# Kernel tuning notes

Hardware: AMD Instinct MI355X
Metric: run time of the kernel (lower is better)

Reference implementation:

```python
import jax, jax.numpy as jnp
import numpy as np

H, HD, NKV = 16, 128, 4           # heads, head_dim, n_kv_heads (kv_groups=4)
SEL_TOPK, SEL_DIM, SEL_HEADS = 64, 64, 1
ROPE_BASE = 10000.0


def _rope_emb(t, hd):
    inv = 1.0 / (ROPE_BASE ** (jnp.arange(0, hd, 2, dtype=jnp.float32) / hd))
    freqs = jnp.arange(t, dtype=jnp.float32)[:, None] * inv[None, :]
    return jnp.concatenate([freqs, freqs], axis=-1)  # [t, hd]


def _apply_rotary(x, rope):
    # x: [b, t, h, hd]; rope: [t, hd] (rot_dim == hd here)
    cos = jnp.cos(rope)[None, :, None, :]
    sin = jnp.sin(rope)[None, :, None, :]
    x1, x2 = x[..., ::2], x[..., 1::2]
    c, s = cos[..., ::2], sin[..., ::2]
    rot = jnp.stack([x1 * c - x2 * s, x1 * s + x2 * c], axis=-1)
    return rot.reshape(x.shape)


def _selector_mask(q, k):
    # q, k: [b, H, t, hd] in UNrotated form (selector_rope='none'); causal=True
    b, h, t, d = q.shape
    qs = q[:, :SEL_HEADS, :, :SEL_DIM]
    ks = k[:, :SEL_HEADS, :, :SEL_DIM]
    scores = jnp.einsum('bhqd,bhkd->bhqk', qs, ks) / np.sqrt(SEL_DIM).astype(np.float32)
    future = jnp.triu(jnp.ones((t, t), bool), 1)
    scores = jnp.where(future[None, None], -jnp.inf, scores)
    idx = jax.lax.top_k(scores, SEL_TOPK)[1]  # [b, h_sel, t, keep]
    rows = jnp.arange(t)
    scatter_row = lambda im: jnp.zeros((t, t), bool).at[rows[:, None], im].set(True)
    sel = jax.vmap(jax.vmap(scatter_row))(idx)          # [b, h_sel, t, t]
    sel = sel.at[:, :, rows, rows].set(True)            # diagonal always kept
    sel = sel & jnp.tril(jnp.ones((t, t), bool))[None, None]
    sel = jnp.any(sel, axis=1, keepdims=True)           # h_sel < h -> broadcast mask
    return jnp.where(sel, 0.0, -jnp.inf).astype(jnp.float32)


def reference(x, Wq, bq, Wkd, bkd, Wku, bku, Wo, bo):
    b, t, d = x.shape
    G = H // NKV
    q = (x @ Wq + bq).reshape(b, t, H, HD)
    kv = (x @ Wkd + bkd) @ Wku + bku                    # MLA: down then up projection
    k = kv[..., : NKV * HD].reshape(b, t, NKV, HD)
    v = kv[..., NKV * HD:].reshape(b, t, NKV, HD)
    rope = _rope_emb(t, HD)
    qb = _apply_rotary(q, rope).transpose(0, 2, 1, 3)                     # [b,H,t,hd]
    kb = jnp.repeat(_apply_rotary(k, rope).transpose(0, 2, 1, 3), G, 1)   # GQA expand
    vb = jnp.repeat(v.transpose(0, 2, 1, 3), G, 1)
    # selector mask from unrotated q/k, detached (selector_detach=True)
    qu = jax.lax.stop_gradient(q.transpose(0, 2, 1, 3))
    ku = jnp.repeat(jax.lax.stop_gradient(k.transpose(0, 2, 1, 3)), G, 1)
    mask = _selector_mask(qu, ku)                                         # [b,1,t,t]
    scores = jnp.einsum('bhqd,bhkd->bhqk', qb, kb) / np.sqrt(HD).astype(np.float32)
    attn = jax.nn.softmax(scores + mask, axis=-1)
    y = jnp.einsum('bhqk,bhkd->bhqd', attn, vb)
    y = y.transpose(0, 2, 1, 3).reshape(b, t, H * HD)
    return y @ Wo + bo


def setup_inputs() -> dict:
    key = jax.random.key(0)
    ks = jax.random.split(key, 6)
    B, T, D, LAT = 2, 2048, 2048, 512
    s = 0.02
    return {
        'x': jax.random.normal(ks[0], (B, T, D), jnp.float32),
        'Wq': jax.random.normal(ks[1], (D, H * HD), jnp.float32) * s,
        'bq': jnp.zeros((H * HD,), jnp.float32),
        'Wkd': jax.random.normal(ks[2], (D, LAT), jnp.float32) * s,
        'bkd': jnp.zeros((LAT,), jnp.float32),
        'Wku': jax.random.normal(ks[3], (LAT, 2 * NKV * HD), jnp.float32) * s,
        'bku': jnp.zeros((2 * NKV * HD,), jnp.float32),
        'Wo': jax.random.normal(ks[4], (H * HD, D), jnp.float32) * s,
        'bo': jnp.zeros((D,), jnp.float32),
    }
```

## Files before the change

kernel.cpp:

```cpp
#include <hip/hip_runtime.h>

typedef unsigned int u32;
typedef unsigned long long u64;
typedef _Float16 f16;
typedef __attribute__((ext_vector_type(2))) _Float16 f16x2;
typedef __attribute__((ext_vector_type(4))) _Float16 f16x4;
typedef __attribute__((ext_vector_type(8))) _Float16 f16x8;
typedef __attribute__((ext_vector_type(4))) float f32x4;
typedef __attribute__((ext_vector_type(2))) double f64x2;


__device__ __forceinline__ int suX(int jj) { return jj ^ ((jj >> 4) & 7); }

__device__ __forceinline__ void dev_transpose_cast(char* smem, int bx, int by,
                                                   const float* __restrict__ in,
                                                   f16* __restrict__ out, int R, int C)
{
  float* tile = (float*)smem;
  int c0 = bx * 32, r0 = by * 32;
  int tx = threadIdx.x & 31, ty = threadIdx.x >> 5;
  #pragma unroll
  for (int i = ty; i < 32; i += 8) tile[i * 33 + tx] = in[(size_t)(r0 + i) * C + c0 + tx];
  __syncthreads();
  #pragma unroll
  for (int i = ty; i < 32; i += 8) out[(size_t)(c0 + i) * R + r0 + tx] = (f16)tile[tx * 33 + i];
}

__global__ __launch_bounds__(256) void k_fusedP(const float* __restrict__ Wq, f16* __restrict__ WqT,
                                                const float* __restrict__ Wkd, f16* __restrict__ WkdT,
                                                const float* __restrict__ Wku, f16* __restrict__ WkuT,
                                                const float* __restrict__ Wo, f16* __restrict__ WoT,
                                                const float* __restrict__ x, f16* __restrict__ xh)
{
  __shared__ __align__(16) char smem[4224];
  const int id = blockIdx.x;
  if (id < 4096) {
    dev_transpose_cast(smem, id & 63, id >> 6, Wq, WqT, 2048, 2048);
  } else if (id < 5120) {
    int g = id - 4096;
    dev_transpose_cast(smem, g & 15, g >> 4, Wkd, WkdT, 2048, 512);
  } else if (id < 5632) {
    int g = id - 5120;
    dev_transpose_cast(smem, g & 31, g >> 5, Wku, WkuT, 512, 1024);
  } else if (id < 9728) {
    int g = id - 5632;
    dev_transpose_cast(smem, g & 63, g >> 6, Wo, WoT, 2048, 2048);
  } else {
    int i = (id - 9728) * 256 + threadIdx.x;
    f32x4 v = *(const f32x4*)&x[(size_t)i * 4];
    f16x4 h; h.x = (f16)v.x; h.y = (f16)v.y; h.z = (f16)v.z; h.w = (f16)v.w;
    *(f16x4*)&xh[(size_t)i * 4] = h;
  }
}

__global__ void k_prep_sel(const float* __restrict__ Wq, const float* __restrict__ Wkd,
                           const float* __restrict__ Wku, double* __restrict__ Bsel)
{
  const int k = blockIdx.x;
  const int j = threadIdx.x;
  Bsel[(size_t)k * 128 + j] = (double)Wq[(size_t)k * 2048 + j];
  double s = 0.0;
  for (int l = 0; l < 512; ++l)
    s = fma((double)Wkd[(size_t)k * 512 + l], (double)Wku[(size_t)l * 1024 + j], s);
  Bsel[(size_t)k * 128 + 64 + j] = s;
}

__global__ void k_bias_sel(const float* __restrict__ bq, const float* __restrict__ bkd,
                           const float* __restrict__ Wku, const float* __restrict__ bku,
                           double* __restrict__ bsel)
{
  int j = threadIdx.x;
  if (j < 64) {
    bsel[j] = (double)bq[j];
  } else {
    int jj = j - 64;
    double s = (double)bku[jj];
    for (int l = 0; l < 512; ++l)
      s = fma((double)bkd[l], (double)Wku[(size_t)l * 1024 + jj], s);
    bsel[j] = s;
  }
}

__device__ __forceinline__ void dev_sel_f64(char* smem, int bx, int by, int bz,
                                            const float* __restrict__ A,
                                            const double* __restrict__ Bsel,
                                            double* __restrict__ partial)
{
  double* Asd = (double*)smem;
  double* Bsd = (double*)smem + 32 * 33;
  const int m0 = bx * 32, n0 = by * 64;
  const int kbase = bz * 256, kend = kbase + 256;
  const int tid = threadIdx.x;
  const int tx = tid & 15, ty = tid >> 4;
  const int ar = tid >> 3, ac4 = (tid & 7) * 4;
  double acc[2][4] = {};

  f32x4 aN = *(const f32x4*)&A[(size_t)(m0 + ar) * 2048 + kbase + ac4];
  f64x2 bN[4];
  #pragma unroll
  for (int it = 0; it < 4; ++it) {
    int c = it * 256 + tid; int kk = c >> 5, n2 = (c & 31) * 2;
    bN[it] = *(const f64x2*)&Bsel[(size_t)(kbase + kk) * 128 + n0 + n2];
  }
  for (int k0 = kbase; k0 < kend; k0 += 32) {
    __syncthreads();
    Asd[ar * 33 + ac4] = (double)aN.x; Asd[ar * 33 + ac4 + 1] = (double)aN.y;
    Asd[ar * 33 + ac4 + 2] = (double)aN.z; Asd[ar * 33 + ac4 + 3] = (double)aN.w;
    #pragma unroll
    for (int it = 0; it < 4; ++it) {
      int c = it * 256 + tid; int kk = c >> 5, n2 = (c & 31) * 2;
      Bsd[kk * 66 + n2] = bN[it].x; Bsd[kk * 66 + n2 + 1] = bN[it].y;
    }
    __syncthreads();
    if (k0 + 32 < kend) {
      aN = *(const f32x4*)&A[(size_t)(m0 + ar) * 2048 + k0 + 32 + ac4];
      #pragma unroll
      for (int it = 0; it < 4; ++it) {
        int c = it * 256 + tid; int kk = c >> 5, n2 = (c & 31) * 2;
        bN[it] = *(const f64x2*)&Bsel[(size_t)(k0 + 32 + kk) * 128 + n0 + n2];
      }
    }
    #pragma unroll
    for (int kk = 0; kk < 32; ++kk) {
      double a0 = Asd[(ty * 2) * 33 + kk], a1 = Asd[(ty * 2 + 1) * 33 + kk];
      f64x2 b01 = *(const f64x2*)&Bsd[kk * 66 + tx * 2];
      f64x2 b23 = *(const f64x2*)&Bsd[kk * 66 + tx * 2 + 32];
      acc[0][0] = fma(a0, b01.x, acc[0][0]); acc[0][1] = fma(a0, b01.y, acc[0][1]);
      acc[0][2] = fma(a0, b23.x, acc[0][2]); acc[0][3] = fma(a0, b23.y, acc[0][3]);
      acc[1][0] = fma(a1, b01.x, acc[1][0]); acc[1][1] = fma(a1, b01.y, acc[1][1]);
      acc[1][2] = fma(a1, b23.x, acc[1][2]); acc[1][3] = fma(a1, b23.y, acc[1][3]);
    }
  }
  double* op = partial + (size_t)bz * 4096 * 128;
  #pragma unroll
  for (int i = 0; i < 2; ++i) {
    int row = m0 + ty * 2 + i;
    #pragma unroll
    for (int j = 0; j < 2; ++j) {
      op[(size_t)row * 128 + n0 + tx * 2 + j] = acc[i][j];
      op[(size_t)row * 128 + n0 + tx * 2 + 32 + j] = acc[i][j + 2];
    }
  }
}

__device__ __forceinline__ void dev_sel_reduce(int blk,
                                               const double* __restrict__ partial,
                                               const double* __restrict__ bias,
                                               double* __restrict__ qs64,
                                               double* __restrict__ ks64)
{
  const int idx = blk * 256 + threadIdx.x;
  const int row = idx >> 7, n = idx & 127;
  const size_t S = 4096 * 128;
  double v = partial[idx];
  #pragma unroll
  for (int z = 1; z < 8; ++z) v += partial[(size_t)z * S + idx];
  v += bias[n];
  if (n < 64) qs64[(size_t)row * 64 + n] = v;
  else        ks64[(size_t)row * 64 + (n - 64)] = v;
}

__global__ __launch_bounds__(256) void k_transpose64(const double* __restrict__ in,
                                                     double* __restrict__ out)
{
  __shared__ double tile[32][33];
  const int bt = blockIdx.z;
  const int c0 = blockIdx.x * 32;
  const int r0 = blockIdx.y * 32;
  int tx = threadIdx.x & 31, ty = threadIdx.x >> 5;
  const double* ip = in + (size_t)bt * 2048 * 64;
  double* op = out + (size_t)bt * 64 * 2048;
  #pragma unroll
  for (int i = ty; i < 32; i += 8) tile[i][tx] = ip[(size_t)(r0 + i) * 64 + c0 + tx];
  __syncthreads();
  #pragma unroll
  for (int i = ty; i < 32; i += 8) op[(size_t)(c0 + i) * 2048 + r0 + tx] = tile[tx][i];
}

__global__ __launch_bounds__(256) void k_score(const double* __restrict__ qs,
                                               const double* __restrict__ ksT,
                                               u64* __restrict__ su)
{
  const int rt = blockIdx.x >> 2;
  const int kc = blockIdx.x & 3;
  const int tmax = ((rt & 63) << 5) + 31;
  if (kc * 512 > tmax) return;
  const int b = rt >> 6;
  const int tid = threadIdx.x;
  __shared__ double As[32 * 64];
  {
    const double* qp = qs + (size_t)rt * 32 * 64;
    #pragma unroll
    for (int i = 0; i < 8; ++i) As[tid * 8 + i] = qp[tid * 8 + i];
  }
  __syncthreads();
  const int k0 = kc * 512 + tid;
  const int k1 = k0 + 256;
  const double* kb = ksT + (size_t)b * 64 * 2048;
  double acc0[32] = {}, acc1[32] = {};
  for (int d = 0; d < 64; ++d) {
    const double b0 = kb[(size_t)d * 2048 + k0];
    const double b1 = kb[(size_t)d * 2048 + k1];
    #pragma unroll
    for (int r = 0; r < 32; ++r) {
      const double a = As[r * 64 + d];
      acc0[r] = fma(a, b0, acc0[r]);
      acc1[r] = fma(a, b1, acc1[r]);
    }
  }
  #pragma unroll
  for (int r = 0; r < 32; ++r) {
    const int row = rt * 32 + r;
    u64 u0 = (u64)__double_as_longlong(acc0[r]);
    u0 = (u0 >> 63) ? ~u0 : (u0 | 0x8000000000000000ull);
    su[(size_t)row * 2048 + k0] = u0;
    u64 u1 = (u64)__double_as_longlong(acc1[r]);
    u1 = (u1 >> 63) ? ~u1 : (u1 | 0x8000000000000000ull);
    su[(size_t)row * 2048 + k1] = u1;
  }
}

template <int MODE>
__device__ __forceinline__ void dev_gemm_bt(char* smem, int gbx, int gby, int nbx, int nby,
                                            const f16* __restrict__ A,
                                            const f16* __restrict__ BT,
                                            const float* __restrict__ bias,
                                            float* __restrict__ C, f16* __restrict__ Ch,
                                            f16* __restrict__ Kout, f16* __restrict__ Vout,
                                            const float* __restrict__ rc,
                                            const float* __restrict__ rs,
                                            int K, int lda, int ldb, int ldc)
{
  f16* As = (f16*)smem;
  f16* Bs = (f16*)smem + 128 * 64;
  const int tid = threadIdx.x;
  const int lane = tid & 63;
  const int wave = tid >> 6;
  int bx = gbx, by = gby;
  {
    const int nwg = nbx * nby;
    if ((nwg & 7) == 0) {
      const int bid = by * nbx + bx;
      const int cpx = nwg >> 3;
      const int sbid = (bid & 7) * cpx + (bid >> 3);
      bx = sbid % nbx;
      by = sbid / nbx;
    }
  }
  const int m0 = bx * 128, n0 = by * 64;
  const int wr = (wave >> 1) * 64, wc = (wave & 1) * 32;
  const int lrow = lane & 15;
  const int kgrp = (lane >> 4) * 8;
  f32x4 acc[4][2] = {};

  for (int k0 = 0; k0 < K; k0 += 64) {
    __syncthreads();
    #pragma unroll
    for (int it = 0; it < 4; ++it) {
      int c = it * 256 + tid;
      int r = c >> 3, c8 = (c & 7) * 8;
      int lbase = (it * 256 + (tid & 192)) * 8;
      const f16* ga = A + (size_t)(m0 + r) * lda + k0 + c8;
      __builtin_amdgcn_global_load_lds((const __attribute__((address_space(1))) u32*)ga,
                                       (__attribute__((address_space(3))) u32*)&As[lbase],
                                       16, 0, 0);
    }
    #pragma unroll
    for (int it = 0; it < 2; ++it) {
      int c = it * 256 + tid;
      int r = c >> 3, c8 = (c & 7) * 8;
      int lbase = (it * 256 + (tid & 192)) * 8;
      const f16* gb = BT + (size_t)(n0 + r) * ldb + k0 + c8;
      __builtin_amdgcn_global_load_lds((const __attribute__((address_space(1))) u32*)gb,
                                       (__attribute__((address_space(3))) u32*)&Bs[lbase],
                                       16, 0, 0);
    }
    __syncthreads();
    #pragma unroll
    for (int ks = 0; ks < 2; ++ks) {
      f16x8 af[4], bfr[2];
      #pragma unroll
      for (int m = 0; m < 4; ++m)
        af[m] = *(const f16x8*)&As[(wr + m * 16 + lrow) * 64 + ks * 32 + kgrp];
      #pragma unroll
      for (int n = 0; n < 2; ++n)
        bfr[n] = *(const f16x8*)&Bs[(wc + n * 16 + lrow) * 64 + ks * 32 + kgrp];
      #pragma unroll
      for (int m = 0; m < 4; ++m)
        #pragma unroll
        for (int n = 0; n < 2; ++n)
          acc[m][n] = __builtin_amdgcn_mfma_f32_16x16x32_f16(af[m], bfr[n], acc[m][n], 0, 0, 0);
    }
  }
  const int rbase = m0 + wr + (lane >> 4) * 4;
  #pragma unroll
  for (int n = 0; n < 2; ++n) {
    int col = n0 + wc + n * 16 + lrow;
    float bv = bias ? bias[col] : 0.0f;
    const int ri = (col & 127) >> 1;
    #pragma unroll
    for (int m = 0; m < 4; ++m) {
      #pragma unroll
      for (int j = 0; j < 4; ++j) {
        int rowi = rbase + m * 16 + j;
        float v = acc[m][n][j] + bv;
        if (MODE == 0) {
          C[(size_t)rowi * ldc + col] = v;
        } else if (MODE == 1) {
          Ch[(size_t)rowi * ldc + col] = (f16)v;
        } else if (MODE == 2) {
          float vp = __shfl_xor(v, 1);
          int t = rowi & 2047;
          float c_ = rc[t * 64 + ri], s_ = rs[t * 64 + ri];
          float r_ = (lrow & 1) ? (vp * s_ + v * c_) : (v * c_ - vp * s_);
          Ch[(size_t)rowi * ldc + col] = (f16)r_;
        } else {
          float vp = __shfl_xor(v, 1);
          if (n0 < 512) {
            int t = rowi & 2047;
            float c_ = rc[t * 64 + ri], s_ = rs[t * 64 + ri];
            float r_ = (lrow & 1) ? (vp * s_ + v * c_) : (v * c_ - vp * s_);
            Kout[(size_t)rowi * 512 + col] = (f16)r_;
          } else {
            Vout[(size_t)rowi * 512 + (col - 512)] = (f16)v;
          }
        }
      }
    }
  }
}

__global__ void k_rope_table(float* __restrict__ rc, float* __restrict__ rs)
{
  int t = blockIdx.x, i = threadIdx.x;
  int fi = (2 * i) & 63;
  double inv = pow(10000.0, -(double)fi / 64.0);
  double a = (double)t * inv;
  rc[t * 64 + i] = (float)cos(a);
  rs[t * 64 + i] = (float)sin(a);
}

__global__ __launch_bounds__(512) void k_select(const u64* __restrict__ gsu,
                                                int* __restrict__ selcnt,
                                                int* __restrict__ selidx)
{
  const int r0 = blockIdx.x * 2;
  const int t0 = r0 & 2047, t1 = t0 + 1;
  const int tid = threadIdx.x;
  const int lane = tid & 63, wave = tid >> 6;
  if (t1 < 64) {
    for (int lr = 0; lr < 2; ++lr) {
      int t = t0 + lr;
      int* outp = selidx + (size_t)(r0 + lr) * 68;
      for (int jj = tid; jj <= t; jj += 512) outp[jj] = jj;
      if (tid == 0) selcnt[r0 + lr] = t + 1;
    }
    return;
  }
  __shared__ u64 su[2][2048];
  __shared__ unsigned hist[256];
  __shared__ unsigned wsum[8];
  __shared__ unsigned s_bsel, s_larger, s_cnt;
  __shared__ u64 s_thr;
  __shared__ int s_remfin;
  __shared__ int cand[128];
  __shared__ u64 ckey[128];

  {
    const u64* g0 = gsu + (size_t)r0 * 2048;
    const u64* g1 = gsu + (size_t)(r0 + 1) * 2048;
    for (int jj = tid; jj <= t1; jj += 512) {
      const int sx = suX(jj);
      if (jj <= t0) su[0][sx] = g0[jj];
      su[1][sx] = g1[jj];
    }
  }
  __syncthreads();

  const int c0 = tid * 4;
  for (int lr = 0; lr < 2; ++lr) {
    const int t = t0 + lr;
    int* outp = selidx + (size_t)(r0 + lr) * 68;
    const u64* S = su[lr];
    u64 kv[4]; bool kvv[4];
    #pragma unroll
    for (int e = 0; e < 4; ++e) {
      const int jj = c0 + e;
      kvv[e] = (jj <= t);
      kv[e] = kvv[e] ? S[suX(jj)] : 0;
    }

    u64 prefix = 0;
    int remaining = 64;
    int broke = 0, sh_final = 0;
    for (int byte = 7; byte >= 0; --byte) {
      const int sh = byte * 8;
      if (tid < 256) hist[tid] = 0;
      __syncthreads();
      {
        unsigned bn[4]; bool vl[4];
        #pragma unroll
        for (int e = 0; e < 4; ++e) {
          vl[e] = kvv[e] && ((byte == 7) || (((kv[e] ^ prefix) >> (sh + 8)) == 0));
          bn[e] = (unsigned)((kv[e] >> sh) & 255);
        }
        unsigned myBin = 0xFFFFFFFFu, cntLoc = 0;
        bool localSame = true;
        #pragma unroll
        for (int e = 0; e < 4; ++e) {
          if (vl[e]) {
            if (myBin == 0xFFFFFFFFu) myBin = bn[e];
            else if (bn[e] != myBin) localSame = false;
            ++cntLoc;
          }
        }
        const bool hasValid = (cntLoc > 0);
        unsigned vmin = hasValid ? myBin : 0xFFFFFFFFu;
        unsigned vmax = hasValid ? myBin : 0u;
        unsigned csum = cntLoc;
        #pragma unroll
        for (int off = 32; off; off >>= 1) {
          unsigned a = __shfl_xor(vmin, off); vmin = a < vmin ? a : vmin;
          unsigned bmx = __shfl_xor(vmax, off); vmax = bmx > vmax ? bmx : vmax;
          csum += __shfl_xor(csum, off);
        }
        const bool anyMixed = (__ballot(hasValid && !localSame) != 0ull);
        const bool anyValid = (__ballot(hasValid) != 0ull);
        if (!anyMixed && anyValid && vmin == vmax) {
          if (lane == 0) atomicAdd(&hist[vmin], csum);
        } else if (hasValid) {
          #pragma unroll
          for (int e = 0; e < 4; ++e) {
            if (vl[e]) {
              bool first = true;
              #pragma unroll
              for (int p = 0; p < 4; ++p)
                if (p < e && vl[p] && bn[p] == bn[e]) first = false;
              if (first) {
                unsigned c = 0;
                #pragma unroll
                for (int q = 0; q < 4; ++q)
                  if (q >= e && vl[q] && bn[q] == bn[e]) ++c;
                atomicAdd(&hist[bn[e]], c);
              }
            }
          }
        }
      }
      __syncthreads();
      unsigned inc = 0, cumAbove = 0;
      if (tid < 256) {
        const unsigned h = hist[tid];
        unsigned v = h;
        #pragma unroll
        for (int off = 1; off < 64; off <<= 1) {
          unsigned tv = __shfl_down(v, off);
          if (lane + off < 64) v += tv;
        }
        if (lane == 0) wsum[wave] = v;
        inc = v; cumAbove = h;
      }
      __syncthreads();
      if (tid < 256) {
        unsigned add = 0;
        #pragma unroll
        for (int w = 0; w < 4; ++w)
          if (w > wave) add += wsum[w];
        const unsigned h = cumAbove;
        inc += add;
        cumAbove = inc - h;
      }
      __syncthreads();
      if (tid < 256 && (int)cumAbove < remaining && (int)inc >= remaining) {
        s_bsel = (unsigned)tid;
        s_larger = cumAbove;
        s_cnt = inc - cumAbove;
      }
      __syncthreads();
      prefix |= ((u64)s_bsel << sh);
      remaining -= (int)s_larger;
      int cnt = (int)s_cnt;
      if (cnt <= 128) { broke = 1; sh_final = sh; break; }
    }
    u64 thr;
    int remfin;
    if (broke) {
      unsigned cg = 0;
      #pragma unroll
      for (int e = 0; e < 4; ++e)
        if (kvv[e] && (((kv[e] ^ prefix) >> sh_final) == 0)) ++cg;
      unsigned v = cg;
      #pragma unroll
      for (int off = 1; off < 64; off <<= 1) {
        unsigned tv = __shfl_up(v, off);
        if (lane >= off) v += tv;
      }
      __syncthreads();
      if (lane == 63) wsum[wave] = v;
      __syncthreads();
      unsigned add = 0, tot = 0;
      #pragma unroll
      for (int w = 0; w < 8; ++w) {
        tot += wsum[w];
        if (w < wave) add += wsum[w];
      }
      const int C = (int)tot;
      int pos = (int)(v + add - cg);
      __syncthreads();
      #pragma unroll
      for (int e = 0; e < 4; ++e)
        if (kvv[e] && (((kv[e] ^ prefix) >> sh_final) == 0)) cand[pos++] = c0 + e;
      __syncthreads();
      if (tid < C) ckey[tid] = S[suX(cand[tid])];
      __syncthreads();
      if (tid < C) {
        u64 k = ckey[tid];
        int g = 0, eq = 0;
        for (int j = 0; j < C; ++j) {
          g += (ckey[j] > k) ? 1 : 0;
          eq += (ckey[j] == k) ? 1 : 0;
        }
        if (g < remaining && remaining <= g + eq) {
          s_thr = k;
          s_remfin = remaining - g;
        }
      }
      __syncthreads();
      thr = s_thr;
      remfin = s_remfin;
    } else {
      thr = prefix;
      remfin = remaining;
    }
    __syncthreads();
    unsigned cg = 0, ct_ = 0;
    #pragma unroll
    for (int e = 0; e < 4; ++e) {
      if (kvv[e]) {
        cg += (kv[e] > thr) ? 1u : 0u;
        ct_ += (kv[e] == thr) ? 1u : 0u;
      }
    }
    const unsigned pack = cg | (ct_ << 16);
    {
      unsigned v = pack;
      #pragma unroll
      for (int off = 1; off < 64; off <<= 1) {
        unsigned tv = __shfl_up(v, off);
        if (lane >= off) v += tv;
      }
      if (lane == 63) wsum[wave] = v;
      __syncthreads();
      unsigned add = 0, tot = 0;
      #pragma unroll
      for (int w = 0; w < 8; ++w) {
        tot += wsum[w];
        if (w < wave) add += wsum[w];
      }
      const unsigned excl = v + add - pack;
      __syncthreads();
      const unsigned Gtot = tot & 0xFFFFu;
      const u64 ut = S[suX(t)];
      const unsigned gt = (ut > thr) ? 1u : 0u;
      const unsigned tt = (ut == thr) ? 1u : 0u;
      const int GtotX = (int)(Gtot - gt);
      int gpos = (int)(excl & 0xFFFFu);
      int tpos = (int)(excl >> 16);
      #pragma unroll
      for (int e = 0; e < 4; ++e) {
        const int jj = c0 + e;
        if (!kvv[e]) break;
        if (kv[e] > thr) {
          if (jj != t) outp[1 + gpos] = jj;
          ++gpos;
        } else if (kv[e] == thr) {
          if (jj != t && tpos < remfin) outp[1 + GtotX + tpos] = jj;
          ++tpos;
        }
      }
      if (tid == 0) {
        outp[0] = t;
        const unsigned Ttot = tot >> 16;
        int tb = (int)(Ttot - tt);
        int emitT = tb < remfin ? tb : remfin;
        selcnt[r0 + lr] = 1 + GtotX + emitT;
      }
    }
    __syncthreads();
  }
}

__global__ __launch_bounds__(256) void k_fusedA(const float* __restrict__ x,
                                                const double* __restrict__ Bsel,
                                                double* __restrict__ partial,
                                                const f16* __restrict__ xh,
                                                const f16* __restrict__ WkdT,
                                                const float* __restrict__ bkd,
                                                f16* __restrict__ cbf)
{
  __shared__ __align__(16) char smem[25600];
  const int id = blockIdx.x;
  if (id < 2048) {
    dev_sel_f64(smem, id & 127, (id >> 7) & 1, id >> 8, x, Bsel, partial);
  } else {
    const int g = id - 2048;
    dev_gemm_bt<1>(smem, g & 31, g >> 5, 32, 8, xh, WkdT, bkd, nullptr, cbf,
                   nullptr, nullptr, nullptr, nullptr, 2048, 2048, 2048, 512);
  }
}

__global__ __launch_bounds__(256) void k_fusedC(const f16* __restrict__ cbf,
                                                const f16* __restrict__ WkuT,
                                                const float* __restrict__ bku,
                                                f16* __restrict__ krope, f16* __restrict__ vbf,
                                                const float* __restrict__ rc,
                                                const float* __restrict__ rs,
                                                const double* __restrict__ partial,
                                                const double* __restrict__ bsel,
                                                double* __restrict__ qs64,
                                                double* __restrict__ ks64)
{
  __shared__ __align__(16) char smem[24576];
  const int id = blockIdx.x;
  if (id < 512) {
    dev_gemm_bt<3>(smem, id & 31, id >> 5, 32, 16, cbf, WkuT, bku, nullptr, nullptr,
                   krope, vbf, rc, rs, 512, 512, 512, 1024);
  } else {
    dev_sel_reduce(id - 512, partial, bsel, qs64, ks64);
  }
}

__global__ __launch_bounds__(256) void k_gemmQ(const f16* __restrict__ xh,
                                               const f16* __restrict__ WqT,
                                               const float* __restrict__ bq,
                                               f16* __restrict__ qrope,
                                               const float* __restrict__ rc,
                                               const float* __restrict__ rs)
{
  __shared__ __align__(16) char smem[24576];
  dev_gemm_bt<2>(smem, blockIdx.x, blockIdx.y, 32, 32, xh, WqT, bq, nullptr, qrope,
                 nullptr, nullptr, rc, rs, 2048, 2048, 2048, 2048);
}

__global__ __launch_bounds__(256) void k_gemmO(const f16* __restrict__ A,
                                               const f16* __restrict__ BT,
                                               const float* __restrict__ bias,
                                               float* __restrict__ C)
{
  __shared__ __align__(16) char smem[24576];
  dev_gemm_bt<0>(smem, blockIdx.x, blockIdx.y, 32, 32, A, BT, bias, C, nullptr,
                 nullptr, nullptr, nullptr, nullptr, 2048, 2048, 2048, 2048);
}

__global__ __launch_bounds__(256) void k_attn(const f16* __restrict__ qr,
                                              const f16* __restrict__ kr,
                                              const f16* __restrict__ vv,
                                              const int* __restrict__ selcnt,
                                              const int* __restrict__ selidx,
                                              f16* __restrict__ y)
{
  const int blk = blockIdx.x;
  const int row = blk >> 2, kvh = blk & 3;
  const int b = row >> 11;
  const int tid = threadIdx.x, lane = tid & 63, wave = tid >> 6;
  const int cnt = selcnt[row];
  __shared__ int sidx[68];
  __shared__ __align__(16) f16 Kl[65 * 128];
  __shared__ __align__(16) f16 Vl[68 * 128];
  __shared__ f16 qlds[4][128];
  __shared__ __align__(4) f16 ph[4][72];
  if (tid < cnt) sidx[tid] = selidx[(size_t)row * 68 + tid];
  *(f16x2*)&qlds[wave][lane * 2] =
      *(const f16x2*)&qr[((size_t)row * 16 + kvh * 4 + wave) * 128 + lane * 2];
  __syncthreads();

  f16x8 kreg[5], vreg[5];
  int rr[5], cc[5]; bool vld[5];
  #pragma unroll
  for (int it = 0; it < 5; ++it) {
    const int c = it * 256 + tid;
    const int r = c >> 4, ch = c & 15;
    const bool ok = (r < cnt);
    const int rsafe = ok ? sidx[r] : sidx[0];
    const size_t kbase = ((size_t)(b * 2048 + rsafe)) * 512 + kvh * 128 + ch * 8;
    kreg[it] = *(const f16x8*)&kr[kbase];
    vreg[it] = *(const f16x8*)&vv[kbase];
    rr[it] = r; cc[it] = ch; vld[it] = ok;
  }
  #pragma unroll
  for (int it = 0; it < 5; ++it) {
    if (vld[it]) {
      *(f16x8*)&Kl[rr[it] * 128 + ((cc[it] ^ (rr[it] & 15)) * 8)] = kreg[it];
      *(f16x8*)&Vl[rr[it] * 128 + cc[it] * 8] = vreg[it];
    }
  }
  for (int i = tid; i < (68 - cnt) * 64; i += 256)
    ((u32*)Vl)[cnt * 64 + i] = 0u;
  __syncthreads();

  const float SCALE = 0.08838834764831845f;
  auto dotk = [&](int r) -> float {
    const int sw = r & 15;
    float s = 0.0f;
    #pragma unroll
    for (int i = 0; i < 16; ++i) {
      f16x8 k8 = *(const f16x8*)&Kl[r * 128 + ((i ^ sw) * 8)];
      f16x8 q8 = *(const f16x8*)&qlds[wave][i * 8];
      #pragma unroll
      for (int e = 0; e < 4; ++e) {
        f16x2 ka; ka.x = k8[2 * e]; ka.y = k8[2 * e + 1];
        f16x2 qa; qa.x = q8[2 * e]; qa.y = q8[2 * e + 1];
        s = __builtin_amdgcn_fdot2(ka, qa, s, false);
      }
    }
    return s * SCALE;
  };

  float s1 = -__builtin_inff(), s2 = -__builtin_inff();
  if (lane < cnt) s1 = dotk(lane);
  if (lane + 64 < cnt) s2 = dotk(lane + 64);
  float mx = fmaxf(s1, s2);
  #pragma unroll
  for (int off = 32; off; off >>= 1) mx = fmaxf(mx, __shfl_xor(mx, off));
  float p1 = (lane < cnt) ? __expf(s1 - mx) : 0.0f;
  float p2 = (lane + 64 < cnt) ? __expf(s2 - mx) : 0.0f;
  float l = p1 + p2;
  #pragma unroll
  for (int off = 32; off; off >>= 1) l += __shfl_xor(l, off);
  float linv = 1.0f / l;
  ph[wave][lane] = (f16)p1;
  if (lane == 0) ph[wave][64] = (f16)p2;
  if (lane >= 1 && lane < 8) ph[wave][64 + lane] = (f16)0.f;
  __syncthreads();

  float y0 = 0.0f, y1 = 0.0f;
  const int d2 = lane * 2;
  for (int j = 0; j < cnt; j += 2) {
    f16x2 pp = *(const f16x2*)&ph[wave][j];
    f16x2 va = *(const f16x2*)&Vl[(j + 0) * 128 + d2];
    f16x2 vb = *(const f16x2*)&Vl[(j + 1) * 128 + d2];
    f16x2 v0; v0.x = va.x; v0.y = vb.x;
    f16x2 v1; v1.x = va.y; v1.y = vb.y;
    y0 = __builtin_amdgcn_fdot2(pp, v0, y0, false);
    y1 = __builtin_amdgcn_fdot2(pp, v1, y1, false);
  }
  y0 *= linv; y1 *= linv;
  f16x2 o; o.x = (f16)y0; o.y = (f16)y1;
  *(f16x2*)&y[(size_t)row * 2048 + (kvh * 4 + wave) * 128 + d2] = o;
}

extern "C" void kernel_launch(void* const* d_in, const int* in_sizes, int n_in,
                              void* d_out, int out_size, void* d_ws, size_t ws_size,
                              hipStream_t stream)
{
  (void)in_sizes; (void)n_in; (void)out_size; (void)ws_size;
  const float* x   = (const float*)d_in[0];
  const float* Wq  = (const float*)d_in[1];
  const float* bq  = (const float*)d_in[2];
  const float* Wkd = (const float*)d_in[3];
  const float* bkd = (const float*)d_in[4];
  const float* Wku = (const float*)d_in[5];
  const float* bku = (const float*)d_in[6];
  const float* Wo  = (const float*)d_in[7];
  const float* bo  = (const float*)d_in[8];
  float* out = (float*)d_out;

  char* ws = (char*)d_ws;
  size_t o = 0;
  auto alloc = [&](size_t bytes) -> void* {
    o = (o + 255) & ~(size_t)255;
    void* p = ws + o;
    o += bytes;
    return p;
  };
  f16* WqT   = (f16*)alloc(2048ull * 2048 * 2);
  f16* WoT   = (f16*)alloc(2048ull * 2048 * 2);
  f16* WkdT  = (f16*)alloc(512ull * 2048 * 2);
  f16* WkuT  = (f16*)alloc(1024ull * 512 * 2);
  f16* xh    = (f16*)alloc(4096ull * 2048 * 2);
  f16* yh    = (f16*)alloc(4096ull * 2048 * 2);
  f16* cbf   = (f16*)alloc(4096ull * 512 * 2);
  float* rc  = (float*)alloc(2048ull * 64 * 4);
  float* rs  = (float*)alloc(2048ull * 64 * 4);
  f16* qrope = (f16*)alloc(4096ull * 2048 * 2);
  f16* krope = (f16*)alloc(4096ull * 512 * 2);
  f16* vbf   = (f16*)alloc(4096ull * 512 * 2);
  int* selcnt = (int*)alloc(4096ull * 4);
  int* selidx = (int*)alloc(4096ull * 68 * 4);
  double* Bsel = (double*)alloc(2048ull * 128 * 8);
  double* bsel = (double*)alloc(128 * 8);
  double* qs64 = (double*)alloc(4096ull * 64 * 8);
  double* ks64 = (double*)alloc(4096ull * 64 * 8);
  double* ksT  = (double*)alloc(2ull * 64 * 2048 * 8);
  double* partial = (double*)alloc(8ull * 4096 * 128 * 8);
  u64* gsu = (u64*)alloc(4096ull * 2048 * 8);

  k_prep_sel<<<2048, 64, 0, stream>>>(Wq, Wkd, Wku, Bsel);
  k_bias_sel<<<1, 128, 0, stream>>>(bq, bkd, Wku, bku, bsel);
  k_rope_table<<<2048, 64, 0, stream>>>(rc, rs);
  k_fusedP<<<17920, 256, 0, stream>>>(Wq, WqT, Wkd, WkdT, Wku, WkuT, Wo, WoT, x, xh);

  k_fusedA<<<2304, 256, 0, stream>>>(x, Bsel, partial, xh, WkdT, bkd, cbf);

  k_fusedC<<<2560, 256, 0, stream>>>(cbf, WkuT, bku, krope, vbf, rc, rs,
                                     partial, bsel, qs64, ks64);

  k_transpose64<<<dim3(2, 64, 2), 256, 0, stream>>>(ks64, ksT);
  k_score<<<512, 256, 0, stream>>>(qs64, ksT, gsu);

  k_gemmQ<<<dim3(32, 32), 256, 0, stream>>>(xh, WqT, bq, qrope, rc, rs);
  k_select<<<2048, 512, 0, stream>>>(gsu, selcnt, selidx);

  k_attn<<<16384, 256, 0, stream>>>(qrope, krope, vbf, selcnt, selidx, yh);

  k_gemmO<<<dim3(32, 32), 256, 0, stream>>>(yh, WoT, bo, out);
}
```

Measured before the change: 492.4 us.

## Merge prep kernels, co-schedule score with Q GEMM, retile select and attn q

Folds the selector-weight prep, selector bias and rope-table kernels into the single preprocessing launch, which removes several small launches. The selector score kernel is retiled to 16-row blocks and launched in the same grid as the Q projection GEMM, so the two independent stages can overlap on the GPU. Top-k selection moves from two rows per 512-thread block to one row per 256-thread block with 8 keys per thread. Attention now keeps the query vector in registers instead of LDS. The trade-off is higher register pressure in the attention and select kernels, and a heterogeneous grid whose shared memory and register use is sized for the larger GEMM path.

```diff
diff --git a/kernel.cpp b/kernel.cpp
--- a/kernel.cpp
+++ b/kernel.cpp
@@ -26,14 +26,21 @@
   for (int i = ty; i < 32; i += 8) out[(size_t)(c0 + i) * R + r0 + tx] = (f16)tile[tx * 33 + i];
 }
 
-__global__ __launch_bounds__(256) void k_fusedP(const float* __restrict__ Wq, f16* __restrict__ WqT,
-                                                const float* __restrict__ Wkd, f16* __restrict__ WkdT,
-                                                const float* __restrict__ Wku, f16* __restrict__ WkuT,
-                                                const float* __restrict__ Wo, f16* __restrict__ WoT,
-                                                const float* __restrict__ x, f16* __restrict__ xh)
+__global__ __launch_bounds__(256) void k_megaP(const float* __restrict__ Wq, f16* __restrict__ WqT,
+                                               const float* __restrict__ Wkd, f16* __restrict__ WkdT,
+                                               const float* __restrict__ Wku, f16* __restrict__ WkuT,
+                                               const float* __restrict__ Wo, f16* __restrict__ WoT,
+                                               const float* __restrict__ x, f16* __restrict__ xh,
+                                               double* __restrict__ Bsel,
+                                               const float* __restrict__ bq,
+                                               const float* __restrict__ bkd,
+                                               const float* __restrict__ bku,
+                                               double* __restrict__ bsel,
+                                               float* __restrict__ rc, float* __restrict__ rs)
 {
   __shared__ __align__(16) char smem[4224];
   const int id = blockIdx.x;
+  const int tid = threadIdx.x;
   if (id < 4096) {
     dev_transpose_cast(smem, id & 63, id >> 6, Wq, WqT, 2048, 2048);
   } else if (id < 5120) {
@@ -45,39 +52,40 @@
   } else if (id < 9728) {
     int g = id - 5632;
     dev_transpose_cast(smem, g & 63, g >> 6, Wo, WoT, 2048, 2048);
-  } else {
-    int i = (id - 9728) * 256 + threadIdx.x;
+  } else if (id < 17920) {
+    int i = (id - 9728) * 256 + tid;
     f32x4 v = *(const f32x4*)&x[(size_t)i * 4];
     f16x4 h; h.x = (f16)v.x; h.y = (f16)v.y; h.z = (f16)v.z; h.w = (f16)v.w;
     *(f16x4*)&xh[(size_t)i * 4] = h;
-  }
-}
-
-__global__ void k_prep_sel(const float* __restrict__ Wq, const float* __restrict__ Wkd,
-                           const float* __restrict__ Wku, double* __restrict__ Bsel)
-{
-  const int k = blockIdx.x;
-  const int j = threadIdx.x;
-  Bsel[(size_t)k * 128 + j] = (double)Wq[(size_t)k * 2048 + j];
-  double s = 0.0;
-  for (int l = 0; l < 512; ++l)
-    s = fma((double)Wkd[(size_t)k * 512 + l], (double)Wku[(size_t)l * 1024 + j], s);
-  Bsel[(size_t)k * 128 + 64 + j] = s;
-}
-
-__global__ void k_bias_sel(const float* __restrict__ bq, const float* __restrict__ bkd,
-                           const float* __restrict__ Wku, const float* __restrict__ bku,
-                           double* __restrict__ bsel)
-{
-  int j = threadIdx.x;
-  if (j < 64) {
-    bsel[j] = (double)bq[j];
+  } else if (id < 18432) {
+    const int k = (id - 17920) * 4 + (tid >> 6);
+    const int j = tid & 63;
+    Bsel[(size_t)k * 128 + j] = (double)Wq[(size_t)k * 2048 + j];
+    double s = 0.0;
+    for (int l = 0; l < 512; ++l)
+      s = fma((double)Wkd[(size_t)k * 512 + l], (double)Wku[(size_t)l * 1024 + j], s);
+    Bsel[(size_t)k * 128 + 64 + j] = s;
+  } else if (id == 18432) {
+    if (tid < 128) {
+      int j = tid;
+      if (j < 64) {
+        bsel[j] = (double)bq[j];
+      } else {
+        int jj = j - 64;
+        double s = (double)bku[jj];
+        for (int l = 0; l < 512; ++l)
+          s = fma((double)bkd[l], (double)Wku[(size_t)l * 1024 + jj], s);
+        bsel[j] = s;
+      }
+    }
   } else {
-    int jj = j - 64;
-    double s = (double)bku[jj];
-    for (int l = 0; l < 512; ++l)
-      s = fma((double)bkd[l], (double)Wku[(size_t)l * 1024 + jj], s);
-    bsel[j] = s;
+    const int t = (id - 18433) * 4 + (tid >> 6);
+    const int i = tid & 63;
+    int fi = (2 * i) & 63;
+    double inv = pow(10000.0, -(double)fi / 64.0);
+    double a = (double)t * inv;
+    rc[t * 64 + i] = (float)cos(a);
+    rs[t * 64 + i] = (float)sin(a);
   }
 }
 
@@ -177,40 +185,41 @@
   for (int i = ty; i < 32; i += 8) op[(size_t)(c0 + i) * 2048 + r0 + tx] = tile[tx][i];
 }
 
-__global__ __launch_bounds__(256) void k_score(const double* __restrict__ qs,
-                                               const double* __restrict__ ksT,
-                                               u64* __restrict__ su)
-{
-  const int rt = blockIdx.x >> 2;
-  const int kc = blockIdx.x & 3;
-  const int tmax = ((rt & 63) << 5) + 31;
+__device__ __forceinline__ void dev_score(char* smem, int sc,
+                                          const double* __restrict__ qs,
+                                          const double* __restrict__ ksT,
+                                          u64* __restrict__ su)
+{
+  const int rt = sc >> 2;
+  const int kc = sc & 3;
+  const int tmax = ((rt & 127) << 4) + 15;
   if (kc * 512 > tmax) return;
-  const int b = rt >> 6;
+  const int b = rt >> 7;
   const int tid = threadIdx.x;
-  __shared__ double As[32 * 64];
+  double* As = (double*)smem;
   {
-    const double* qp = qs + (size_t)rt * 32 * 64;
-    #pragma unroll
-    for (int i = 0; i < 8; ++i) As[tid * 8 + i] = qp[tid * 8 + i];
+    const double* qp = qs + (size_t)rt * 16 * 64;
+    #pragma unroll
+    for (int i = 0; i < 4; ++i) As[tid * 4 + i] = qp[tid * 4 + i];
   }
   __syncthreads();
   const int k0 = kc * 512 + tid;
   const int k1 = k0 + 256;
   const double* kb = ksT + (size_t)b * 64 * 2048;
-  double acc0[32] = {}, acc1[32] = {};
+  double acc0[16] = {}, acc1[16] = {};
   for (int d = 0; d < 64; ++d) {
     const double b0 = kb[(size_t)d * 2048 + k0];
     const double b1 = kb[(size_t)d * 2048 + k1];
     #pragma unroll
-    for (int r = 0; r < 32; ++r) {
+    for (int r = 0; r < 16; ++r) {
       const double a = As[r * 64 + d];
       acc0[r] = fma(a, b0, acc0[r]);
       acc1[r] = fma(a, b1, acc1[r]);
     }
   }
   #pragma unroll
-  for (int r = 0; r < 32; ++r) {
-    const int row = rt * 32 + r;
+  for (int r = 0; r < 16; ++r) {
+    const int row = rt * 16 + r;
     u64 u0 = (u64)__double_as_longlong(acc0[r]);
     u0 = (u0 >> 63) ? ~u0 : (u0 | 0x8000000000000000ull);
     su[(size_t)row * 2048 + k0] = u0;
@@ -330,266 +339,6 @@
   }
 }
 
-__global__ void k_rope_table(float* __restrict__ rc, float* __restrict__ rs)
-{
-  int t = blockIdx.x, i = threadIdx.x;
-  int fi = (2 * i) & 63;
-  double inv = pow(10000.0, -(double)fi / 64.0);
-  double a = (double)t * inv;
-  rc[t * 64 + i] = (float)cos(a);
-  rs[t * 64 + i] = (float)sin(a);
-}
-
-__global__ __launch_bounds__(512) void k_select(const u64* __restrict__ gsu,
-                                                int* __restrict__ selcnt,
-                                                int* __restrict__ selidx)
-{
-  const int r0 = blockIdx.x * 2;
-  const int t0 = r0 & 2047, t1 = t0 + 1;
-  const int tid = threadIdx.x;
-  const int lane = tid & 63, wave = tid >> 6;
-  if (t1 < 64) {
-    for (int lr = 0; lr < 2; ++lr) {
-      int t = t0 + lr;
-      int* outp = selidx + (size_t)(r0 + lr) * 68;
-      for (int jj = tid; jj <= t; jj += 512) outp[jj] = jj;
-      if (tid == 0) selcnt[r0 + lr] = t + 1;
-    }
-    return;
-  }
-  __shared__ u64 su[2][2048];
-  __shared__ unsigned hist[256];
-  __shared__ unsigned wsum[8];
-  __shared__ unsigned s_bsel, s_larger, s_cnt;
-  __shared__ u64 s_thr;
-  __shared__ int s_remfin;
-  __shared__ int cand[128];
-  __shared__ u64 ckey[128];
-
-  {
-    const u64* g0 = gsu + (size_t)r0 * 2048;
-    const u64* g1 = gsu + (size_t)(r0 + 1) * 2048;
-    for (int jj = tid; jj <= t1; jj += 512) {
-      const int sx = suX(jj);
-      if (jj <= t0) su[0][sx] = g0[jj];
-      su[1][sx] = g1[jj];
-    }
-  }
-  __syncthreads();
-
-  const int c0 = tid * 4;
-  for (int lr = 0; lr < 2; ++lr) {
-    const int t = t0 + lr;
-    int* outp = selidx + (size_t)(r0 + lr) * 68;
-    const u64* S = su[lr];
-    u64 kv[4]; bool kvv[4];
-    #pragma unroll
-    for (int e = 0; e < 4; ++e) {
-      const int jj = c0 + e;
-      kvv[e] = (jj <= t);
-      kv[e] = kvv[e] ? S[suX(jj)] : 0;
-    }
-
-    u64 prefix = 0;
-    int remaining = 64;
-    int broke = 0, sh_final = 0;
-    for (int byte = 7; byte >= 0; --byte) {
-      const int sh = byte * 8;
-      if (tid < 256) hist[tid] = 0;
-      __syncthreads();
-      {
-        unsigned bn[4]; bool vl[4];
-        #pragma unroll
-        for (int e = 0; e < 4; ++e) {
-          vl[e] = kvv[e] && ((byte == 7) || (((kv[e] ^ prefix) >> (sh + 8)) == 0));
-          bn[e] = (unsigned)((kv[e] >> sh) & 255);
-        }
-        unsigned myBin = 0xFFFFFFFFu, cntLoc = 0;
-        bool localSame = true;
-        #pragma unroll
-        for (int e = 0; e < 4; ++e) {
-          if (vl[e]) {
-            if (myBin == 0xFFFFFFFFu) myBin = bn[e];
-            else if (bn[e] != myBin) localSame = false;
-            ++cntLoc;
-          }
-        }
-        const bool hasValid = (cntLoc > 0);
-        unsigned vmin = hasValid ? myBin : 0xFFFFFFFFu;
-        unsigned vmax = hasValid ? myBin : 0u;
-        unsigned csum = cntLoc;
-        #pragma unroll
-        for (int off = 32; off; off >>= 1) {
-          unsigned a = __shfl_xor(vmin, off); vmin = a < vmin ? a : vmin;
-          unsigned bmx = __shfl_xor(vmax, off); vmax = bmx > vmax ? bmx : vmax;
-          csum += __shfl_xor(csum, off);
-        }
-        const bool anyMixed = (__ballot(hasValid && !localSame) != 0ull);
-        const bool anyValid = (__ballot(hasValid) != 0ull);
-        if (!anyMixed && anyValid && vmin == vmax) {
-          if (lane == 0) atomicAdd(&hist[vmin], csum);
-        } else if (hasValid) {
-          #pragma unroll
-          for (int e = 0; e < 4; ++e) {
-            if (vl[e]) {
-              bool first = true;
-              #pragma unroll
-              for (int p = 0; p < 4; ++p)
-                if (p < e && vl[p] && bn[p] == bn[e]) first = false;
-              if (first) {
-                unsigned c = 0;
-                #pragma unroll
-                for (int q = 0; q < 4; ++q)
-                  if (q >= e && vl[q] && bn[q] == bn[e]) ++c;
-                atomicAdd(&hist[bn[e]], c);
-              }
-            }
-          }
-        }
-      }
-      __syncthreads();
-      unsigned inc = 0, cumAbove = 0;
-      if (tid < 256) {
-        const unsigned h = hist[tid];
-        unsigned v = h;
-        #pragma unroll
-        for (int off = 1; off < 64; off <<= 1) {
-          unsigned tv = __shfl_down(v, off);
-          if (lane + off < 64) v += tv;
-        }
-        if (lane == 0) wsum[wave] = v;
-        inc = v; cumAbove = h;
-      }
-      __syncthreads();
-      if (tid < 256) {
-        unsigned add = 0;
-        #pragma unroll
-        for (int w = 0; w < 4; ++w)
-          if (w > wave) add += wsum[w];
-        const unsigned h = cumAbove;
-        inc += add;
-        cumAbove = inc - h;
-      }
-      __syncthreads();
-      if (tid < 256 && (int)cumAbove < remaining && (int)inc >= remaining) {
-        s_bsel = (unsigned)tid;
-        s_larger = cumAbove;
-        s_cnt = inc - cumAbove;
-      }
-      __syncthreads();
-      prefix |= ((u64)s_bsel << sh);
-      remaining -= (int)s_larger;
-      int cnt = (int)s_cnt;
-      if (cnt <= 128) { broke = 1; sh_final = sh; break; }
-    }
-    u64 thr;
-    int remfin;
-    if (broke) {
-      unsigned cg = 0;
-      #pragma unroll
-      for (int e = 0; e < 4; ++e)
-        if (kvv[e] && (((kv[e] ^ prefix) >> sh_final) == 0)) ++cg;
-      unsigned v = cg;
-      #pragma unroll
-      for (int off = 1; off < 64; off <<= 1) {
-        unsigned tv = __shfl_up(v, off);
-        if (lane >= off) v += tv;
-      }
-      __syncthreads();
-      if (lane == 63) wsum[wave] = v;
-      __syncthreads();
-      unsigned add = 0, tot = 0;
-      #pragma unroll
-      for (int w = 0; w < 8; ++w) {
-        tot += wsum[w];
-        if (w < wave) add += wsum[w];
-      }
-      const int C = (int)tot;
-      int pos = (int)(v + add - cg);
-      __syncthreads();
-      #pragma unroll
-      for (int e = 0; e < 4; ++e)
-        if (kvv[e] && (((kv[e] ^ prefix) >> sh_final) == 0)) cand[pos++] = c0 + e;
-      __syncthreads();
-      if (tid < C) ckey[tid] = S[suX(cand[tid])];
-      __syncthreads();
-      if (tid < C) {
-        u64 k = ckey[tid];
-        int g = 0, eq = 0;
-        for (int j = 0; j < C; ++j) {
-          g += (ckey[j] > k) ? 1 : 0;
-          eq += (ckey[j] == k) ? 1 : 0;
-        }
-        if (g < remaining && remaining <= g + eq) {
-          s_thr = k;
-          s_remfin = remaining - g;
-        }
-      }
-      __syncthreads();
-      thr = s_thr;
-      remfin = s_remfin;
-    } else {
-      thr = prefix;
-      remfin = remaining;
-    }
-    __syncthreads();
-    unsigned cg = 0, ct_ = 0;
-    #pragma unroll
-    for (int e = 0; e < 4; ++e) {
-      if (kvv[e]) {
-        cg += (kv[e] > thr) ? 1u : 0u;
-        ct_ += (kv[e] == thr) ? 1u : 0u;
-      }
-    }
-    const unsigned pack = cg | (ct_ << 16);
-    {
-      unsigned v = pack;
-      #pragma unroll
-      for (int off = 1; off < 64; off <<= 1) {
-        unsigned tv = __shfl_up(v, off);
-        if (lane >= off) v += tv;
-      }
-      if (lane == 63) wsum[wave] = v;
-      __syncthreads();
-      unsigned add = 0, tot = 0;
-      #pragma unroll
-      for (int w = 0; w < 8; ++w) {
-        tot += wsum[w];
-        if (w < wave) add += wsum[w];
-      }
-      const unsigned excl = v + add - pack;
-      __syncthreads();
-      const unsigned Gtot = tot & 0xFFFFu;
-      const u64 ut = S[suX(t)];
-      const unsigned gt = (ut > thr) ? 1u : 0u;
-      const unsigned tt = (ut == thr) ? 1u : 0u;
-      const int GtotX = (int)(Gtot - gt);
-      int gpos = (int)(excl & 0xFFFFu);
-      int tpos = (int)(excl >> 16);
-      #pragma unroll
-      for (int e = 0; e < 4; ++e) {
-        const int jj = c0 + e;
-        if (!kvv[e]) break;
-        if (kv[e] > thr) {
-          if (jj != t) outp[1 + gpos] = jj;
-          ++gpos;
-        } else if (kv[e] == thr) {
-          if (jj != t && tpos < remfin) outp[1 + GtotX + tpos] = jj;
-          ++tpos;
-        }
-      }
-      if (tid == 0) {
-        outp[0] = t;
-        const unsigned Ttot = tot >> 16;
-        int tb = (int)(Ttot - tt);
-        int emitT = tb < remfin ? tb : remfin;
-        selcnt[r0 + lr] = 1 + GtotX + emitT;
-      }
-    }
-    __syncthreads();
-  }
-}
-
 __global__ __launch_bounds__(256) void k_fusedA(const float* __restrict__ x,
                                                 const double* __restrict__ Bsel,
                                                 double* __restrict__ partial,
@@ -630,16 +379,24 @@
   }
 }
 
-__global__ __launch_bounds__(256) void k_gemmQ(const f16* __restrict__ xh,
-                                               const f16* __restrict__ WqT,
-                                               const float* __restrict__ bq,
-                                               f16* __restrict__ qrope,
-                                               const float* __restrict__ rc,
-                                               const float* __restrict__ rs)
+__global__ __launch_bounds__(256) void k_fusedQS(const f16* __restrict__ xh,
+                                                 const f16* __restrict__ WqT,
+                                                 const float* __restrict__ bq,
+                                                 f16* __restrict__ qrope,
+                                                 const float* __restrict__ rc,
+                                                 const float* __restrict__ rs,
+                                                 const double* __restrict__ qs64,
+                                                 const double* __restrict__ ksT,
+                                                 u64* __restrict__ gsu)
 {
   __shared__ __align__(16) char smem[24576];
-  dev_gemm_bt<2>(smem, blockIdx.x, blockIdx.y, 32, 32, xh, WqT, bq, nullptr, qrope,
-                 nullptr, nullptr, rc, rs, 2048, 2048, 2048, 2048);
+  const int id = blockIdx.x;
+  if (id < 1024) {
+    dev_gemm_bt<2>(smem, id & 31, id >> 5, 32, 32, xh, WqT, bq, nullptr, qrope,
+                   nullptr, nullptr, rc, rs, 2048, 2048, 2048, 2048);
+  } else {
+    dev_score(smem, id - 1024, qs64, ksT, gsu);
+  }
 }
 
 __global__ __launch_bounds__(256) void k_gemmO(const f16* __restrict__ A,
@@ -650,6 +407,235 @@
   __shared__ __align__(16) char smem[24576];
   dev_gemm_bt<0>(smem, blockIdx.x, blockIdx.y, 32, 32, A, BT, bias, C, nullptr,
                  nullptr, nullptr, nullptr, nullptr, 2048, 2048, 2048, 2048);
+}
+
+__global__ __launch_bounds__(256) void k_select(const u64* __restrict__ gsu,
+                                                int* __restrict__ selcnt,
+                                                int* __restrict__ selidx)
+{
+  const int row = blockIdx.x;
+  const int t = row & 2047;
+  const int tid = threadIdx.x;
+  const int lane = tid & 63, wave = tid >> 6;
+  int* outp = selidx + (size_t)row * 68;
+  if (t < 64) {
+    for (int jj = tid; jj <= t; jj += 256) outp[jj] = jj;
+    if (tid == 0) selcnt[row] = t + 1;
+    return;
+  }
+  __shared__ u64 su[2048];
+  __shared__ unsigned hist[256];
+  __shared__ unsigned wsum[4];
+  __shared__ unsigned s_bsel, s_larger, s_cnt;
+  __shared__ u64 s_thr;
+  __shared__ int s_remfin;
+  __shared__ int cand[128];
+  __shared__ u64 ckey[128];
+
+  {
+    const u64* g = gsu + (size_t)row * 2048;
+    for (int jj = tid; jj <= t; jj += 256) su[suX(jj)] = g[jj];
+  }
+  __syncthreads();
+
+  const int c0 = tid * 8;
+  u64 kv[8]; bool kvv[8];
+  #pragma unroll
+  for (int e = 0; e < 8; ++e) {
+    const int jj = c0 + e;
+    kvv[e] = (jj <= t);
+    kv[e] = kvv[e] ? su[suX(jj)] : 0;
+  }
+
+  u64 prefix = 0;
+  int remaining = 64;
+  int broke = 0, sh_final = 0;
+  for (int byte = 7; byte >= 0; --byte) {
+    const int sh = byte * 8;
+    hist[tid] = 0;
+    __syncthreads();
+    {
+      unsigned bn[8]; bool vl[8];
+      #pragma unroll
+      for (int e = 0; e < 8; ++e) {
+        vl[e] = kvv[e] && ((byte == 7) || (((kv[e] ^ prefix) >> (sh + 8)) == 0));
+        bn[e] = (unsigned)((kv[e] >> sh) & 255);
+      }
+      unsigned myBin = 0xFFFFFFFFu, cntLoc = 0;
+      bool localSame = true;
+      #pragma unroll
+      for (int e = 0; e < 8; ++e) {
+        if (vl[e]) {
+          if (myBin == 0xFFFFFFFFu) myBin = bn[e];
+          else if (bn[e] != myBin) localSame = false;
+          ++cntLoc;
+        }
+      }
+      const bool hasValid = (cntLoc > 0);
+      unsigned vmin = hasValid ? myBin : 0xFFFFFFFFu;
+      unsigned vmax = hasValid ? myBin : 0u;
+      unsigned csum = cntLoc;
+      #pragma unroll
+      for (int off = 32; off; off >>= 1) {
+        unsigned a = __shfl_xor(vmin, off); vmin = a < vmin ? a : vmin;
+        unsigned bmx = __shfl_xor(vmax, off); vmax = bmx > vmax ? bmx : vmax;
+        csum += __shfl_xor(csum, off);
+      }
+      const bool anyMixed = (__ballot(hasValid && !localSame) != 0ull);
+      const bool anyValid = (__ballot(hasValid) != 0ull);
+      if (!anyMixed && anyValid && vmin == vmax) {
+        if (lane == 0) atomicAdd(&hist[vmin], csum);
+      } else if (hasValid) {
+        #pragma unroll
+        for (int e = 0; e < 8; ++e) {
+          if (vl[e]) {
+            bool first = true;
+            #pragma unroll
+            for (int p = 0; p < 8; ++p)
+              if (p < e && vl[p] && bn[p] == bn[e]) first = false;
+            if (first) {
+              unsigned c = 0;
+              #pragma unroll
+              for (int q = 0; q < 8; ++q)
+                if (q >= e && vl[q] && bn[q] == bn[e]) ++c;
+              atomicAdd(&hist[bn[e]], c);
+            }
+          }
+        }
+      }
+    }
+    __syncthreads();
+    const unsigned h = hist[tid];
+    unsigned v = h;
+    #pragma unroll
+    for (int off = 1; off < 64; off <<= 1) {
+      unsigned tv = __shfl_down(v, off);
+      if (lane + off < 64) v += tv;
+    }
+    if (lane == 0) wsum[wave] = v;
+    __syncthreads();
+    unsigned add = 0;
+    #pragma unroll
+    for (int w = 0; w < 4; ++w)
+      if (w > wave) add += wsum[w];
+    const unsigned inc = v + add;
+    const unsigned cumAbove = inc - h;
+    __syncthreads();
+    if ((int)cumAbove < remaining && (int)inc >= remaining) {
+      s_bsel = (unsigned)tid;
+      s_larger = cumAbove;
+      s_cnt = inc - cumAbove;
+    }
+    __syncthreads();
+    prefix |= ((u64)s_bsel << sh);
+    remaining -= (int)s_larger;
+    int cnt = (int)s_cnt;
+    if (cnt <= 128) { broke = 1; sh_final = sh; break; }
+  }
+  u64 thr;
+  int remfin;
+  if (broke) {
+    unsigned cg = 0;
+    #pragma unroll
+    for (int e = 0; e < 8; ++e)
+      if (kvv[e] && (((kv[e] ^ prefix) >> sh_final) == 0)) ++cg;
+    unsigned v = cg;
+    #pragma unroll
+    for (int off = 1; off < 64; off <<= 1) {
+      unsigned tv = __shfl_up(v, off);
+      if (lane >= off) v += tv;
+    }
+    __syncthreads();
+    if (lane == 63) wsum[wave] = v;
+    __syncthreads();
+    unsigned add = 0, tot = 0;
+    #pragma unroll
+    for (int w = 0; w < 4; ++w) {
+      tot += wsum[w];
+      if (w < wave) add += wsum[w];
+    }
+    const int C = (int)tot;
+    int pos = (int)(v + add - cg);
+    __syncthreads();
+    #pragma unroll
+    for (int e = 0; e < 8; ++e)
+      if (kvv[e] && (((kv[e] ^ prefix) >> sh_final) == 0)) cand[pos++] = c0 + e;
+    __syncthreads();
+    if (tid < C) ckey[tid] = su[suX(cand[tid])];
+    __syncthreads();
+    if (tid < C) {
+      u64 k = ckey[tid];
+      int g = 0, eq = 0;
+      for (int j = 0; j < C; ++j) {
+        g += (ckey[j] > k) ? 1 : 0;
+        eq += (ckey[j] == k) ? 1 : 0;
+      }
+      if (g < remaining && remaining <= g + eq) {
+        s_thr = k;
+        s_remfin = remaining - g;
+      }
+    }
+    __syncthreads();
+    thr = s_thr;
+    remfin = s_remfin;
+  } else {
+    thr = prefix;
+    remfin = remaining;
+  }
+  __syncthreads();
+  unsigned cg = 0, ct_ = 0;
+  #pragma unroll
+  for (int e = 0; e < 8; ++e) {
+    if (kvv[e]) {
+      cg += (kv[e] > thr) ? 1u : 0u;
+      ct_ += (kv[e] == thr) ? 1u : 0u;
+    }
+  }
+  const unsigned pack = cg | (ct_ << 16);
+  {
+    unsigned v = pack;
+    #pragma unroll
+    for (int off = 1; off < 64; off <<= 1) {
+      unsigned tv = __shfl_up(v, off);
+      if (lane >= off) v += tv;
+    }
+    if (lane == 63) wsum[wave] = v;
+    __syncthreads();
+    unsigned add = 0, tot = 0;
+    #pragma unroll
+    for (int w = 0; w < 4; ++w) {
+      tot += wsum[w];
+      if (w < wave) add += wsum[w];
+    }
+    const unsigned excl = v + add - pack;
+    __syncthreads();
+    const unsigned Gtot = tot & 0xFFFFu;
+    const u64 ut = su[suX(t)];
+    const unsigned gt = (ut > thr) ? 1u : 0u;
+    const unsigned tt = (ut == thr) ? 1u : 0u;
+    const int GtotX = (int)(Gtot - gt);
+    int gpos = (int)(excl & 0xFFFFu);
+    int tpos = (int)(excl >> 16);
+    #pragma unroll
+    for (int e = 0; e < 8; ++e) {
+      const int jj = c0 + e;
+      if (!kvv[e]) break;
+      if (kv[e] > thr) {
+        if (jj != t) outp[1 + gpos] = jj;
+        ++gpos;
+      } else if (kv[e] == thr) {
+        if (jj != t && tpos < remfin) outp[1 + GtotX + tpos] = jj;
+        ++tpos;
+      }
+    }
+    if (tid == 0) {
+      outp[0] = t;
+      const unsigned Ttot = tot >> 16;
+      int tb = (int)(Ttot - tt);
+      int emitT = tb < remfin ? tb : remfin;
+      selcnt[row] = 1 + GtotX + emitT;
+    }
+  }
 }
 
 __global__ __launch_bounds__(256) void k_attn(const f16* __restrict__ qr,
@@ -667,11 +653,12 @@
   __shared__ int sidx[68];
   __shared__ __align__(16) f16 Kl[65 * 128];
   __shared__ __align__(16) f16 Vl[68 * 128];
-  __shared__ f16 qlds[4][128];
   __shared__ __align__(4) f16 ph[4][72];
   if (tid < cnt) sidx[tid] = selidx[(size_t)row * 68 + tid];
-  *(f16x2*)&qlds[wave][lane * 2] =
-      *(const f16x2*)&qr[((size_t)row * 16 + kvh * 4 + wave) * 128 + lane * 2];
+  const f16* qb = qr + ((size_t)row * 16 + kvh * 4 + wave) * 128;
+  f16x8 qf[16];
+  #pragma unroll
+  for (int i = 0; i < 16; ++i) qf[i] = *(const f16x8*)&qb[i * 8];
   __syncthreads();
 
   f16x8 kreg[5], vreg[5];
@@ -705,7 +692,7 @@
     #pragma unroll
     for (int i = 0; i < 16; ++i) {
       f16x8 k8 = *(const f16x8*)&Kl[r * 128 + ((i ^ sw) * 8)];
-      f16x8 q8 = *(const f16x8*)&qlds[wave][i * 8];
+      f16x8 q8 = qf[i];
       #pragma unroll
       for (int e = 0; e < 4; ++e) {
         f16x2 ka; ka.x = k8[2 * e]; ka.y = k8[2 * e + 1];
@@ -795,10 +782,8 @@
   double* partial = (double*)alloc(8ull * 4096 * 128 * 8);
   u64* gsu = (u64*)alloc(4096ull * 2048 * 8);
 
-  k_prep_sel<<<2048, 64, 0, stream>>>(Wq, Wkd, Wku, Bsel);
-  k_bias_sel<<<1, 128, 0, stream>>>(bq, bkd, Wku, bku, bsel);
-  k_rope_table<<<2048, 64, 0, stream>>>(rc, rs);
-  k_fusedP<<<17920, 256, 0, stream>>>(Wq, WqT, Wkd, WkdT, Wku, WkuT, Wo, WoT, x, xh);
+  k_megaP<<<18945, 256, 0, stream>>>(Wq, WqT, Wkd, WkdT, Wku, WkuT, Wo, WoT, x, xh,
+                                     Bsel, bq, bkd, bku, bsel, rc, rs);
 
   k_fusedA<<<2304, 256, 0, stream>>>(x, Bsel, partial, xh, WkdT, bkd, cbf);
 
@@ -806,10 +791,10 @@
                                      partial, bsel, qs64, ks64);
 
   k_transpose64<<<dim3(2, 64, 2), 256, 0, stream>>>(ks64, ksT);
-  k_score<<<512, 256, 0, stream>>>(qs64, ksT, gsu);
-
-  k_gemmQ<<<dim3(32, 32), 256, 0, stream>>>(xh, WqT, bq, qrope, rc, rs);
-  k_select<<<2048, 512, 0, stream>>>(gsu, selcnt, selidx);
+
+  k_fusedQS<<<2048, 256, 0, stream>>>(xh, WqT, bq, qrope, rc, rs, qs64, ksT, gsu);
+
+  k_select<<<4096, 256, 0, stream>>>(gsu, selcnt, selidx);
 
   k_attn<<<16384, 256, 0, stream>>>(qrope, krope, vbf, selcnt, selidx, yh);
 
```

Result: faster. 481.2 us (-2.3%).
